# Performance work log

Measured on AMD Instinct MI355X. Metric: run time of the kernel, lower is better.

## Reference

```python
import jax, jax.numpy as jnp
import numpy as np

B, S, C, H, L = 256, 8, 8, 501, 56


def _lin_init(k, out_dim, in_dim):
    k1, k2 = jax.random.split(k)
    s = 1.0 / np.sqrt(in_dim)
    w = jax.random.uniform(k1, (out_dim, in_dim), jnp.float32, -s, s)
    b = jax.random.uniform(k2, (out_dim,), jnp.float32, -s, s)
    return w, b


def setup_inputs() -> dict:
    key = jax.random.key(0)
    ks = jax.random.split(key, 12)
    lin1_w, lin1_b = _lin_init(ks[0], H, L)
    av_w1, av_b1 = _lin_init(ks[1], 2 * H, H)
    av_w2, av_b2 = _lin_init(ks[2], C, 2 * H)
    ae_w1, ae_b1 = _lin_init(ks[3], 4 * H, 2 * H)
    ae_w2, ae_b2 = _lin_init(ks[4], 1, 4 * H)
    gate_w, gate_b = _lin_init(ks[5], H, H)
    map_w, map_b = _lin_init(ks[6], H, H)
    gru_w_ih, gru_b_ih = _lin_init(ks[7], 3 * H, C)
    gru_w_hh, gru_b_hh = _lin_init(ks[8], 3 * H, H)
    z = jax.random.normal(ks[9], (B, L), jnp.float32)
    dep_graph = jax.random.uniform(ks[10], (B, S, S), jnp.float32)
    node_encoding = jax.random.uniform(ks[11], (B, S, C), jnp.float32)
    return dict(z=z, dep_graph=dep_graph, node_encoding=node_encoding,
                lin1_w=lin1_w, lin1_b=lin1_b,
                av_w1=av_w1, av_b1=av_b1, av_w2=av_w2, av_b2=av_b2,
                ae_w1=ae_w1, ae_b1=ae_b1, ae_w2=ae_w2, ae_b2=ae_b2,
                gate_w=gate_w, gate_b=gate_b, map_w=map_w, map_b=map_b,
                gru_w_ih=gru_w_ih, gru_w_hh=gru_w_hh,
                gru_b_ih=gru_b_ih, gru_b_hh=gru_b_hh)


def _forward(z, dep_graph, node_encoding,
             lin1_w, lin1_b, av_w1, av_b1, av_w2, av_b2,
             ae_w1, ae_b1, ae_w2, ae_b2, gate_w, gate_b, map_w, map_b,
             gru_w_ih, gru_w_hh, gru_b_ih, gru_b_hh):
    b, s, _ = dep_graph.shape
    h = lin1_w.shape[0]

    def gru(x, hid):  # torch GRUCell math
        gi = x @ gru_w_ih.T + gru_b_ih
        gh = hid @ gru_w_hh.T + gru_b_hh
        i_r, i_z, i_n = jnp.split(gi, 3, axis=-1)
        h_r, h_z, h_n = jnp.split(gh, 3, axis=-1)
        r = jax.nn.sigmoid(i_r + h_r)
        zz = jax.nn.sigmoid(i_z + h_z)
        n = jnp.tanh(i_n + r * h_n)
        return (1.0 - zz) * n + zz * hid

    pos = jnp.arange(s)

    def outer_step(carry, xs):
        graph_state, nhs = carry  # (B,H), (B,S,H)
        index, x, dep_row = xs    # scalar, (B,C), (B,S)
        logits = jax.nn.softmax(
            jax.nn.relu(graph_state @ av_w1.T + av_b1) @ av_w2.T + av_b2, axis=-1)
        # index==0: gru seeded with graph_state; otherwise zero hidden
        h0 = jnp.where(index == 0, graph_state, jnp.zeros_like(graph_state))
        hv0 = gru(x, h0)

        def inner_step(c, j):
            hv, nhs_c, edge_row = c
            active = j < index  # replicate range(index-1, -1, -1)
            hidden_j = nhs_c[:, j]
            e = jnp.concatenate([hv, hidden_j], axis=1)
            edge = (jax.nn.relu(e @ ae_w1.T + ae_b1) @ ae_w2.T + ae_b2)[:, 0]
            edge_row = edge_row.at[:, j].set(jnp.where(active, edge, 0.0))
            # ancestors: dep_graph[:, index] with positions < j zeroed
            anc = dep_row * (pos >= j).astype(dep_row.dtype)
            a = (nhs_c * anc[:, :, None]).reshape(b * s, h)
            h_in = (jax.nn.sigmoid(a @ gate_w.T + gate_b) *
                    (a @ map_w.T + map_b)).reshape(b, s, h).sum(axis=1)
            hv_new = gru(x, h_in)
            hv = jnp.where(active, hv_new, hv)
            nhs_c = nhs_c.at[:, index].set(jnp.where(active, hv_new, nhs_c[:, index]))
            return (hv, nhs_c, edge_row), None

        (hv, nhs, edge_row), _ = jax.lax.scan(
            inner_step, (hv0, nhs, jnp.zeros((b, s), dep_graph.dtype)),
            jnp.arange(s - 1, -1, -1))
        nhs = nhs.at[:, index].set(hv)
        return (hv, nhs), (logits, edge_row)

    graph_state0 = z @ lin1_w.T + lin1_b
    nhs0 = jnp.zeros((b, s, h), z.dtype)
    (_, _), (gen_enc, gen_dep) = jax.lax.scan(
        outer_step, (graph_state0, nhs0),
        (jnp.arange(s), node_encoding.transpose(1, 0, 2), dep_graph.transpose(1, 0, 2)))
    return gen_dep.transpose(1, 0, 2), gen_enc.transpose(1, 0, 2)


def reference(z, dep_graph, node_encoding,
              lin1_w, lin1_b, av_w1, av_b1, av_w2, av_b2,
              ae_w1, ae_b1, ae_w2, ae_b2, gate_w, gate_b, map_w, map_b,
              gru_w_ih, gru_w_hh, gru_b_ih, gru_b_hh):
    return _forward(z, dep_graph, node_encoding,
                    lin1_w, lin1_b, av_w1, av_b1, av_w2, av_b2,
                    ae_w1, ae_b1, ae_w2, ae_b2, gate_w, gate_b, map_w, map_b,
                    gru_w_ih, gru_w_hh, gru_b_ih, gru_b_hh)
```

## Files before the change

kernel.cpp:

```cpp
#include <hip/hip_runtime.h>
#include <math.h>

constexpr int NB  = 256;
constexpr int NS  = 8;
constexpr int NC  = 8;
constexpr int NH  = 501;
constexpr int NL  = 56;
constexpr int NH2 = 1002;
constexpr int NH3 = 1503;
constexpr int NH4 = 2004;
constexpr int KT  = 1536;
constexpr int KE  = 512;
constexpr int KA  = 1024;
constexpr int HV  = 512 * 256;

typedef unsigned short u16;
typedef short bf16x8v __attribute__((ext_vector_type(8)));
typedef _Float16 f16x8v __attribute__((ext_vector_type(8)));
typedef _Float16 f16x4v __attribute__((ext_vector_type(4)));
typedef float f32x4 __attribute__((ext_vector_type(4)));

__device__ __forceinline__ float sigf(float x) { return 1.0f / (1.0f + __expf(-x)); }
__device__ __forceinline__ float tanh2(float x) { return 2.0f * sigf(2.0f * x) - 1.0f; }

__device__ __forceinline__ u16 f2bf(float x) {
  union { float f; unsigned u; } c; c.f = x;
  unsigned r = (c.u + 0x7fffu + ((c.u >> 16) & 1u)) >> 16;
  return (u16)r;
}
__device__ __forceinline__ float bf2f(u16 h) {
  union { float f; unsigned u; } c; c.u = ((unsigned)h) << 16; return c.f;
}

__device__ __forceinline__ void async_copy16(const void* g, void* l) {
  __builtin_amdgcn_global_load_lds(
      (const __attribute__((address_space(1))) unsigned int*)g,
      (__attribute__((address_space(3))) unsigned int*)l, 16, 0, 0);
}

__device__ __forceinline__ f32x4 mfma_bf(bf16x8v a, bf16x8v b, f32x4 c) {
  return __builtin_amdgcn_mfma_f32_16x16x32_bf16(a, b, c, 0, 0, 0);
}
__device__ __forceinline__ f32x4 mfma_h(f16x8v a, f16x8v b, f32x4 c) {
  return __builtin_amdgcn_mfma_f32_16x16x32_f16(a, b, c, 0, 0, 0);
}

__device__ __forceinline__ void storeTrio(u16* __restrict__ T, int b, int h0, const float v[4]) {
  size_t base = (size_t)b * KT;
  if (h0 + 3 < NH) {
    ushort4 hi4, lo4;
    u16 hi, lo;
    hi = f2bf(v[0]); lo = f2bf(v[0] - bf2f(hi)); hi4.x = hi; lo4.x = lo;
    hi = f2bf(v[1]); lo = f2bf(v[1] - bf2f(hi)); hi4.y = hi; lo4.y = lo;
    hi = f2bf(v[2]); lo = f2bf(v[2] - bf2f(hi)); hi4.z = hi; lo4.z = lo;
    hi = f2bf(v[3]); lo = f2bf(v[3] - bf2f(hi)); hi4.w = hi; lo4.w = lo;
    *(ushort4*)&T[base + h0]        = hi4;
    *(ushort4*)&T[base + 512 + h0]  = lo4;
    *(ushort4*)&T[base + 1024 + h0] = hi4;
  } else {
    for (int r = 0; r < 4; ++r) {
      int h = h0 + r;
      if (h < NH) {
        u16 hi = f2bf(v[r]); u16 lo = f2bf(v[r] - bf2f(hi));
        T[base + h] = hi; T[base + 512 + h] = lo; T[base + 1024 + h] = hi;
      }
    }
  }
}

__global__ __launch_bounds__(256) void kPack(
    const float* __restrict__ gate_w, const float* __restrict__ map_w,
    const float* __restrict__ w_hh, const float* __restrict__ av_w1,
    const float* __restrict__ ae_w1,
    u16* __restrict__ Wgm, u16* __restrict__ Whh, u16* __restrict__ Wav1,
    _Float16* __restrict__ Wlr) {
  int r = blockIdx.x;
  if (r < 3584) {
    for (int k = threadIdx.x; k < 512; k += 256) {
      float v = 0.f; u16* dst; int rr;
      if (r < 1024) {
        int h = (r < 512) ? r : r - 512;
        if (h < NH && k < NH) v = (r < 512) ? gate_w[h * NH + k] : map_w[h * NH + k];
        dst = Wgm; rr = r;
      } else if (r < 2560) {
        rr = r - 1024; int g = rr >> 9, h = rr & 511;
        if (h < NH && k < NH) v = w_hh[((size_t)g * NH + h) * NH + k];
        dst = Whh;
      } else {
        rr = r - 2560;
        if (rr < NH2 && k < NH) v = av_w1[(size_t)rr * NH + k];
        dst = Wav1;
      }
      u16 hi = f2bf(v); u16 lo = f2bf(v - bf2f(hi));
      dst[(size_t)rr * KT + k] = hi;
      dst[(size_t)rr * KT + 512 + k] = hi;
      dst[(size_t)rr * KT + 1024 + k] = lo;
    }
  } else {
    int m = r - 3584;
    for (int k = threadIdx.x; k < KA; k += 256) {
      float v = 0.f;
      if (m < NH4) {
        if (k < 512) { if (k < NH) v = ae_w1[(size_t)m * NH2 + k]; }
        else { int kk = k - 512; if (kk < NH) v = ae_w1[(size_t)m * NH2 + NH + kk]; }
      }
      Wlr[(size_t)m * KA + k] = (_Float16)v;
    }
  }
}

__global__ __launch_bounds__(256) void kInit(
    float* __restrict__ out0, const float* __restrict__ ae_b2,
    u16* __restrict__ trio, _Float16* __restrict__ Xe, _Float16* __restrict__ Xn,
    const float* __restrict__ z, const float* __restrict__ lin1_w,
    const float* __restrict__ lin1_b, float* __restrict__ g0,
    const float* __restrict__ ne, const float* __restrict__ w_ih,
    const float* __restrict__ b_ih, float* __restrict__ giN, float* __restrict__ giT) {
  int blk = blockIdx.x, t = threadIdx.x;
  if (blk < 64) {
    int e = blk * 256 + t;
    int b = e >> 6, r = e & 63;
    int i = r >> 3, jj = r & 7;
    out0[b * 64 + i * 8 + jj] = (jj < i) ? ae_b2[0] : 0.f;
  } else if (blk < 75) {
    u16* T = trio + (size_t)(blk - 64) * ((size_t)NB * KT) + (size_t)t * KT;
#pragma unroll
    for (int seg = 0; seg < 3; ++seg)
      for (int h = NH; h < 512; ++h) T[seg * 512 + h] = 0;
  } else if (blk < 103) {
    _Float16* X = Xe + (size_t)(blk - 75) * NB * KE + (size_t)t * KE;
    for (int h = NH; h < 512; ++h) X[h] = (_Float16)0.f;
  } else if (blk < 110) {
    _Float16* X = Xn + (size_t)(blk - 103) * NB * KE + (size_t)t * KE;
    for (int h = NH; h < 512; ++h) X[h] = (_Float16)0.f;
  } else if (blk < 366) {
    int b = blk - 110;
    const float* zr = z + (size_t)b * NL;
    for (int h = t; h < NH; h += 256) {
      const float* wr = lin1_w + (size_t)h * NL;
      float acc = lin1_b[h];
#pragma unroll
      for (int l = 0; l < NL; ++l) acc += zr[l] * wr[l];
      g0[h * NB + b] = acc;
      u16 hi = f2bf(acc), lo = f2bf(acc - bf2f(hi));
      trio[(size_t)b * KT + h] = hi;
      trio[(size_t)b * KT + 512 + h] = lo;
      trio[(size_t)b * KT + 1024 + h] = hi;
    }
  } else {
    int r0 = (blk - 366) * 6, b = t;
    for (int rr = 0; rr < 6; ++rr) {
      int r = r0 + rr;
      if (r >= NH3) break;
      int g = (r >= NH2) ? 2 : ((r >= NH) ? 1 : 0);
      int h = r - g * NH;
      float wv[8];
#pragma unroll
      for (int c = 0; c < 8; ++c) wv[c] = w_ih[r * NC + c];
      float bb = b_ih[r];
      for (int idx = 0; idx < 8; ++idx) {
        float acc = bb;
#pragma unroll
        for (int c = 0; c < 8; ++c) acc += ne[b * 64 + idx * 8 + c] * wv[c];
        giN[((size_t)idx * NH3 + r) * NB + b] = acc;
        giT[((size_t)idx * NB + b) * KT + g * 512 + h] = acc;
      }
    }
  }
}


__global__ __launch_bounds__(512) void kGMT(
    const u16* __restrict__ Wgm, const u16* __restrict__ Bsrc,
    float* __restrict__ PcO, float* __restrict__ QcO,
    const float* __restrict__ dep, const float* __restrict__ gate_b,
    const float* __restrict__ map_b, float* __restrict__ RS, u16* __restrict__ hinT,
    const float* __restrict__ giT, const float* __restrict__ b_hh,
    _Float16* __restrict__ Xe0, int index) {
  __shared__ f32x4 red[8 * 4 * 64];
  const int b = blockIdx.x, t = threadIdx.x, w = t >> 6, l = t & 63;
  const int quad = l >> 4, lan = l & 15;
  const int ht = b & 31, ct = b >> 5;
  const u16* Ag = Wgm + (size_t)(ht * 16 + lan) * KT;
  const u16* Am = Wgm + (size_t)(512 + ht * 16 + lan) * KT;
  const u16* B0 = Bsrc + (size_t)(ct * 32 + lan) * KT;
  const u16* B1 = Bsrc + (size_t)(ct * 32 + 16 + lan) * KT;
  const int kb = w * 192 + quad * 8;
  f32x4 a0 = {0.f,0.f,0.f,0.f}, a1 = a0, a2 = a0, a3 = a0;
#pragma unroll 3
  for (int ks = 0; ks < 6; ++ks) {
    int k = kb + ks * 32;
    bf16x8v bg = *(const bf16x8v*)&B0[k];
    bf16x8v bh = *(const bf16x8v*)&B1[k];
    bf16x8v ag = *(const bf16x8v*)&Ag[k];
    bf16x8v am = *(const bf16x8v*)&Am[k];
    a0 = mfma_bf(ag, bg, a0); a1 = mfma_bf(ag, bh, a1);
    a2 = mfma_bf(am, bg, a2); a3 = mfma_bf(am, bh, a3);
  }
  red[(w * 4 + 0) * 64 + l] = a0;
  red[(w * 4 + 1) * 64 + l] = a1;
  red[(w * 4 + 2) * 64 + l] = a2;
  red[(w * 4 + 3) * 64 + l] = a3;
  __syncthreads();
  if (w < 2) {
    int ns = w;
    f32x4 G = red[(0 * 4 + ns) * 64 + l];
    f32x4 M = red[(0 * 4 + 2 + ns) * 64 + l];
#pragma unroll
    for (int p = 1; p < 8; ++p) {
      G += red[(p * 4 + ns) * 64 + l];
      M += red[(p * 4 + 2 + ns) * 64 + l];
    }
    int c = ct * 32 + ns * 16 + lan;
    int h0 = ht * 16 + quad * 4;
    int j = index - 1;
    float dj = dep[c * 64 + index * 8 + j];
    float vout[4];
#pragma unroll
    for (int reg = 0; reg < 4; ++reg) {
      int h = h0 + reg; float v = 0.f;
      if (h < NH) {
        PcO[h * NB + c] = G[reg];
        QcO[h * NB + c] = M[reg];
        float gb = gate_b[h], mb = map_b[h];
        float kbv = sigf(gb) * mb;
        float fj = sigf(dj * G[reg] + gb) * (dj * M[reg] + mb);
        RS[h * NB + c] = fj;
        v = fj + 7.0f * kbv;
      }
      vout[reg] = v;
    }
    storeTrio(hinT, c, h0, vout);
  } else if (w < 4) {
    int t2 = t - 128;
    int c = ct * 32 + (t2 & 31);
    int hb = t2 >> 5;
    const float* g = giT + ((size_t)index * NB + c) * KT;
#pragma unroll
    for (int k = 0; k < 4; ++k) {
      int h = ht * 16 + hb * 4 + k;
      if (h < NH) {
        float rr = sigf(g[h] + b_hh[h]);
        float zz = sigf(g[512 + h] + b_hh[NH + h]);
        float nn = tanh2(g[1024 + h] + rr * b_hh[2 * NH + h]);
        Xe0[(size_t)c * KE + h] = (_Float16)((1.f - zz) * nn);
      }
    }
  }
}

__global__ __launch_bounds__(512) void kGM0(
    const u16* __restrict__ Wgm, const u16* __restrict__ Bsrc,
    const float* __restrict__ dep, const float* __restrict__ gate_b,
    const float* __restrict__ map_b,
    const float* __restrict__ Pcj, const float* __restrict__ Qcj,
    float* __restrict__ RS, u16* __restrict__ hinT, int index, int j) {
  __shared__ f32x4 red[8 * 4 * 64];
  const int b = blockIdx.x, t = threadIdx.x, w = t >> 6, l = t & 63;
  const int quad = l >> 4, lan = l & 15;
  const int ht = b & 31, ct = b >> 5;
  const u16* Ag = Wgm + (size_t)(ht * 16 + lan) * KT;
  const u16* Am = Wgm + (size_t)(512 + ht * 16 + lan) * KT;
  const u16* B0 = Bsrc + (size_t)(ct * 32 + lan) * KT;
  const u16* B1 = Bsrc + (size_t)(ct * 32 + 16 + lan) * KT;
  const int kb = w * 192 + quad * 8;
  f32x4 a0 = {0.f,0.f,0.f,0.f}, a1 = a0, a2 = a0, a3 = a0;
#pragma unroll 3
  for (int ks = 0; ks < 6; ++ks) {
    int k = kb + ks * 32;
    bf16x8v bg = *(const bf16x8v*)&B0[k];
    bf16x8v bh = *(const bf16x8v*)&B1[k];
    bf16x8v ag = *(const bf16x8v*)&Ag[k];
    bf16x8v am = *(const bf16x8v*)&Am[k];
    a0 = mfma_bf(ag, bg, a0); a1 = mfma_bf(ag, bh, a1);
    a2 = mfma_bf(am, bg, a2); a3 = mfma_bf(am, bh, a3);
  }
  red[(w * 4 + 0) * 64 + l] = a0;
  red[(w * 4 + 1) * 64 + l] = a1;
  red[(w * 4 + 2) * 64 + l] = a2;
  red[(w * 4 + 3) * 64 + l] = a3;
  __syncthreads();
  if (w < 2) {
    int ns = w;
    f32x4 G = red[(0 * 4 + ns) * 64 + l];
    f32x4 M = red[(0 * 4 + 2 + ns) * 64 + l];
#pragma unroll
    for (int p = 1; p < 8; ++p) {
      G += red[(p * 4 + ns) * 64 + l];
      M += red[(p * 4 + 2 + ns) * 64 + l];
    }
    int c = ct * 32 + ns * 16 + lan;
    int h0 = ht * 16 + quad * 4;
    float dj = dep[c * 64 + index * 8 + j];
    float di = dep[c * 64 + index * 8 + index];
    float cnt = (float)(7 - (index - j));
    float vout[4];
#pragma unroll
    for (int reg = 0; reg < 4; ++reg) {
      int h = h0 + reg; float v = 0.f;
      if (h < NH) {
        float gb = gate_b[h], mb = map_b[h];
        float kbv = sigf(gb) * mb;
        float fj = sigf(dj * Pcj[h * NB + c] + gb) * (dj * Qcj[h * NB + c] + mb);
        float rs = RS[h * NB + c] + fj;
        RS[h * NB + c] = rs;
        float fi = sigf(di * G[reg] + gb) * (di * M[reg] + mb);
        v = rs + fi + cnt * kbv;
      }
      vout[reg] = v;
    }
    storeTrio(hinT, c, h0, vout);
  }
}

__global__ __launch_bounds__(512) void kHHw(
    const u16* __restrict__ Whh, const u16* __restrict__ Bsrc,
    const float* __restrict__ hidF, const float* __restrict__ gi,
    const float* __restrict__ b_hh,
    u16* __restrict__ dstT, _Float16* __restrict__ XeSlot, _Float16* __restrict__ XnSlot) {
  __shared__ f32x4 red[8 * 6 * 64];
  const int b = blockIdx.x, t = threadIdx.x, w = t >> 6, l = t & 63;
  const int quad = l >> 4, lan = l & 15;
  const int ht = b & 31, ct = b >> 5;
  const u16* Ar = Whh + (size_t)(ht * 16 + lan) * KT;
  const u16* Az = Whh + (size_t)(512 + ht * 16 + lan) * KT;
  const u16* An = Whh + (size_t)(1024 + ht * 16 + lan) * KT;
  const u16* B0 = Bsrc + (size_t)(ct * 32 + lan) * KT;
  const u16* B1 = Bsrc + (size_t)(ct * 32 + 16 + lan) * KT;
  const int kb = w * 192 + quad * 8;
  f32x4 r0 = {0.f,0.f,0.f,0.f}, r1 = r0, z0 = r0, z1 = r0, n0 = r0, n1 = r0;
#pragma unroll 3
  for (int ks = 0; ks < 6; ++ks) {
    int k = kb + ks * 32;
    bf16x8v bg = *(const bf16x8v*)&B0[k];
    bf16x8v bh = *(const bf16x8v*)&B1[k];
    bf16x8v ar = *(const bf16x8v*)&Ar[k];
    bf16x8v az = *(const bf16x8v*)&Az[k];
    bf16x8v an = *(const bf16x8v*)&An[k];
    r0 = mfma_bf(ar, bg, r0); r1 = mfma_bf(ar, bh, r1);
    z0 = mfma_bf(az, bg, z0); z1 = mfma_bf(az, bh, z1);
    n0 = mfma_bf(an, bg, n0); n1 = mfma_bf(an, bh, n1);
  }
  red[(w * 6 + 0) * 64 + l] = r0;
  red[(w * 6 + 1) * 64 + l] = r1;
  red[(w * 6 + 2) * 64 + l] = z0;
  red[(w * 6 + 3) * 64 + l] = z1;
  red[(w * 6 + 4) * 64 + l] = n0;
  red[(w * 6 + 5) * 64 + l] = n1;
  __syncthreads();
  if (w < 2) {
    int ns = w;
    f32x4 Rr = red[(0 * 6 + 0 + ns) * 64 + l];
    f32x4 Rz = red[(0 * 6 + 2 + ns) * 64 + l];
    f32x4 Rn = red[(0 * 6 + 4 + ns) * 64 + l];
#pragma unroll
    for (int p = 1; p < 8; ++p) {
      Rr += red[(p * 6 + 0 + ns) * 64 + l];
      Rz += red[(p * 6 + 2 + ns) * 64 + l];
      Rn += red[(p * 6 + 4 + ns) * 64 + l];
    }
    int c = ct * 32 + ns * 16 + lan;
    int h0 = ht * 16 + quad * 4;
    float vout[4];
#pragma unroll
    for (int reg = 0; reg < 4; ++reg) {
      int h = h0 + reg; float v = 0.f;
      if (h < NH) {
        float ir = gi[h * NB + c];
        float iz = gi[(NH + h) * NB + c];
        float inn = gi[(2 * NH + h) * NB + c];
        float rr = sigf(ir + Rr[reg] + b_hh[h]);
        float zz = sigf(iz + Rz[reg] + b_hh[NH + h]);
        float nn = tanh2(inn + rr * (Rn[reg] + b_hh[2 * NH + h]));
        float hd;
        if (hidF) hd = hidF[h * NB + c];
        else hd = bf2f(Bsrc[(size_t)c * KT + h]) + bf2f(Bsrc[(size_t)c * KT + 512 + h]);
        v = (1.f - zz) * nn + zz * hd;
      }
      vout[reg] = v;
    }
    storeTrio(dstT, c, h0, vout);
    if (XeSlot || XnSlot) {
      if (h0 + 3 < NH) {
        f16x4v xv; xv[0] = (_Float16)vout[0]; xv[1] = (_Float16)vout[1];
        xv[2] = (_Float16)vout[2]; xv[3] = (_Float16)vout[3];
        if (XeSlot) *(f16x4v*)&XeSlot[(size_t)c * KE + h0] = xv;
        if (XnSlot) *(f16x4v*)&XnSlot[(size_t)c * KE + h0] = xv;
      } else {
        for (int reg = 0; reg < 4; ++reg)
          if (h0 + reg < NH) {
            if (XeSlot) XeSlot[(size_t)c * KE + h0 + reg] = (_Float16)vout[reg];
            if (XnSlot) XnSlot[(size_t)c * KE + h0 + reg] = (_Float16)vout[reg];
          }
      }
    }
  }
}


__global__ __launch_bounds__(256) void kEdge(const _Float16* __restrict__ Wlr,
                                             const _Float16* __restrict__ Xe,
                                             const _Float16* __restrict__ Xn,
                                             const float* __restrict__ ae_b1,
                                             const float* __restrict__ ae_w2,
                                             float* __restrict__ out0) {
  __shared__ u16 sA[2][128 * 32];
  __shared__ u16 sB[2][128 * 32];
  __shared__ float shW[4][8][16];
  const int t = threadIdx.x, w = t >> 6, l = t & 63, quad = l >> 4, lan = l & 15;
  const int mB = blockIdx.x * 128, nB0 = blockIdx.y * 128;
  const int qs = quad ^ ((lan >> 1) & 3);
  const int sseg = (l & 3) ^ ((l >> 3) & 3);
  int sid = blockIdx.y >> 1;
  int idec = 1, bse = 0;
  while (sid >= bse + idec) { bse += idec; idec++; }
  int jdec = idec - 1 - (sid - bse);
  int r0 = (w * 2 + 0) * 16 + (l >> 2), r1 = (w * 2 + 1) * 16 + (l >> 2);
  const _Float16* gA0 = Wlr + (size_t)(mB + r0) * KA + sseg * 8;
  const _Float16* gA1 = Wlr + (size_t)(mB + r1) * KA + sseg * 8;
  const _Float16* Xe0 = Xe + (size_t)(nB0 + r0) * KE + sseg * 8;
  const _Float16* Xe1 = Xe + (size_t)(nB0 + r1) * KE + sseg * 8;
  const _Float16* Xn0 = Xn + ((size_t)jdec * NB + ((nB0 + r0) & 255)) * KE + sseg * 8;
  const _Float16* Xn1 = Xn + ((size_t)jdec * NB + ((nB0 + r1) & 255)) * KE + sseg * 8;
  f32x4 acc[2][8];
#pragma unroll
  for (int mt = 0; mt < 2; ++mt)
#pragma unroll
    for (int ns = 0; ns < 8; ++ns) acc[mt][ns] = (f32x4){0.f,0.f,0.f,0.f};
  async_copy16(gA0, &sA[0][(w * 2 + 0) * 512]);
  async_copy16(gA1, &sA[0][(w * 2 + 1) * 512]);
  async_copy16(Xe0, &sB[0][(w * 2 + 0) * 512]);
  async_copy16(Xe1, &sB[0][(w * 2 + 1) * 512]);
  for (int c = 0; c < 32; ++c) {
    __syncthreads();
    if (c + 1 < 32) {
      int nb = (c + 1) & 1, cc = c + 1;
      async_copy16(gA0 + cc * 32, &sA[nb][(w * 2 + 0) * 512]);
      async_copy16(gA1 + cc * 32, &sA[nb][(w * 2 + 1) * 512]);
      const _Float16* b0 = (cc < 16) ? (Xe0 + cc * 32) : (Xn0 + (cc - 16) * 32);
      const _Float16* b1 = (cc < 16) ? (Xe1 + cc * 32) : (Xn1 + (cc - 16) * 32);
      async_copy16(b0, &sB[nb][(w * 2 + 0) * 512]);
      async_copy16(b1, &sB[nb][(w * 2 + 1) * 512]);
    }
    const u16* bufA = sA[c & 1];
    const u16* bufB = sB[c & 1];
    f16x8v av[2];
#pragma unroll
    for (int mt = 0; mt < 2; ++mt)
      av[mt] = *(const f16x8v*)&bufA[(w * 32 + mt * 16 + lan) * 32 + qs * 8];
#pragma unroll
    for (int ns = 0; ns < 8; ++ns) {
      f16x8v bv = *(const f16x8v*)&bufB[(ns * 16 + lan) * 32 + qs * 8];
#pragma unroll
      for (int mt = 0; mt < 2; ++mt) acc[mt][ns] = mfma_h(av[mt], bv, acc[mt][ns]);
    }
  }
  float b1v[2][4], w2v[2][4];
#pragma unroll
  for (int mt = 0; mt < 2; ++mt) {
    int m0 = mB + w * 32 + mt * 16 + quad * 4;
#pragma unroll
    for (int reg = 0; reg < 4; ++reg) {
      int m = m0 + reg;
      b1v[mt][reg] = (m < NH4) ? ae_b1[m] : 0.f;
      w2v[mt][reg] = (m < NH4) ? ae_w2[m] : 0.f;
    }
  }
#pragma unroll
  for (int ns = 0; ns < 8; ++ns) {
    float s = 0.f;
#pragma unroll
    for (int mt = 0; mt < 2; ++mt) {
#pragma unroll
      for (int reg = 0; reg < 4; ++reg) {
        float v = acc[mt][ns][reg] + b1v[mt][reg];
        if (v > 0.f) s += v * w2v[mt][reg];
      }
    }
    s += __shfl_xor(s, 16);
    s += __shfl_xor(s, 32);
    if (quad == 0) shW[w][ns][lan] = s;
  }
  __syncthreads();
  if (t < 128) {
    int ns = t >> 4, ln = t & 15;
    float tot = shW[0][ns][ln] + shW[1][ns][ln] + shW[2][ns][ln] + shW[3][ns][ln];
    int b = (nB0 + ln + ns * 16) & 255;
    atomicAdd(&out0[b * 64 + idec * 8 + jdec], tot);
  }
}

__global__ __launch_bounds__(256) void kLogA(const u16* __restrict__ Wav1,
                                             const u16* __restrict__ Bsrc,
                                             const float* __restrict__ av_b1,
                                             _Float16* __restrict__ t1) {
  __shared__ u16 sA[2][64 * 32];
  __shared__ u16 sB[2][128 * 32];
  const int t = threadIdx.x, w = t >> 6, l = t & 63, quad = l >> 4, lan = l & 15;
  const int mB = blockIdx.x * 64, nB0 = blockIdx.y * 128;
  const int qs = quad ^ ((lan >> 1) & 3);
  const int sseg = (l & 3) ^ ((l >> 3) & 3);
  int rA = w * 16 + (l >> 2);
  int r0 = (w * 2 + 0) * 16 + (l >> 2), r1 = (w * 2 + 1) * 16 + (l >> 2);
  const u16* gA = Wav1 + (size_t)(mB + rA) * KT + sseg * 8;
  const u16* gB0 = Bsrc + (size_t)(nB0 + r0) * KT + sseg * 8;
  const u16* gB1 = Bsrc + (size_t)(nB0 + r1) * KT + sseg * 8;
  f32x4 acc[8];
#pragma unroll
  for (int ns = 0; ns < 8; ++ns) acc[ns] = (f32x4){0.f,0.f,0.f,0.f};
  async_copy16(gA, &sA[0][w * 512]);
  async_copy16(gB0, &sB[0][(w * 2 + 0) * 512]);
  async_copy16(gB1, &sB[0][(w * 2 + 1) * 512]);
  for (int c = 0; c < 48; ++c) {
    __syncthreads();
    if (c + 1 < 48) {
      int nb = (c + 1) & 1, off = (c + 1) * 32;
      async_copy16(gA + off, &sA[nb][w * 512]);
      async_copy16(gB0 + off, &sB[nb][(w * 2 + 0) * 512]);
      async_copy16(gB1 + off, &sB[nb][(w * 2 + 1) * 512]);
    }
    const u16* bufA = sA[c & 1];
    const u16* bufB = sB[c & 1];
    bf16x8v av = *(const bf16x8v*)&bufA[(w * 16 + lan) * 32 + qs * 8];
#pragma unroll
    for (int ns = 0; ns < 8; ++ns) {
      bf16x8v bv = *(const bf16x8v*)&bufB[(ns * 16 + lan) * 32 + qs * 8];
      acc[ns] = mfma_bf(av, bv, acc[ns]);
    }
  }
#pragma unroll
  for (int ns = 0; ns < 8; ++ns) {
    int col = nB0 + ns * 16 + lan;
    int m0 = mB + w * 16 + quad * 4;
    f16x4v rv;
#pragma unroll
    for (int reg = 0; reg < 4; ++reg) {
      int m = m0 + reg;
      float v = acc[ns][reg] + ((m < NH2) ? av_b1[m] : 0.f);
      rv[reg] = (_Float16)(v > 0.f ? v : 0.f);
    }
    *(f16x4v*)&t1[(size_t)col * 1024 + m0] = rv;
  }
}

__global__ __launch_bounds__(256) void kSoft(const _Float16* __restrict__ t1,
                                             const float* __restrict__ av_w2,
                                             const float* __restrict__ av_b2,
                                             float* __restrict__ out1) {
  const int t = threadIdx.x, w = t >> 6, l = t & 63;
  int col = blockIdx.x * 4 + w;
  const _Float16* trow = t1 + (size_t)col * 1024;
  float s[8] = {};
  for (int i = 0; i < 16; ++i) {
    int k = i * 64 + l;
    if (k < NH2) {
      float v = (float)trow[k];
#pragma unroll
      for (int c = 0; c < 8; ++c) s[c] += v * av_w2[c * NH2 + k];
    }
  }
#pragma unroll
  for (int c = 0; c < 8; ++c) {
    s[c] += __shfl_xor(s[c], 32);
    s[c] += __shfl_xor(s[c], 16);
    s[c] += __shfl_xor(s[c], 8);
    s[c] += __shfl_xor(s[c], 4);
    s[c] += __shfl_xor(s[c], 2);
    s[c] += __shfl_xor(s[c], 1);
  }
  if (l == 0) {
    float lg[8], mx = -1e30f;
#pragma unroll
    for (int c = 0; c < 8; ++c) { lg[c] = s[c] + av_b2[c]; mx = fmaxf(mx, lg[c]); }
    float den = 0.f;
#pragma unroll
    for (int c = 0; c < 8; ++c) den += __expf(lg[c] - mx);
    int idx = col >> 8, b = col & 255;
#pragma unroll
    for (int c = 0; c < 8; ++c)
      out1[(b * NS + idx) * NC + c] = __expf(lg[c] - mx) / den;
  }
}


extern "C" void kernel_launch(void* const* d_in, const int* in_sizes, int n_in,
                              void* d_out, int out_size, void* d_ws, size_t ws_size,
                              hipStream_t stream) {
  (void)in_sizes; (void)n_in; (void)out_size; (void)ws_size;
  const float* z      = (const float*)d_in[0];
  const float* dep    = (const float*)d_in[1];
  const float* ne     = (const float*)d_in[2];
  const float* lin1_w = (const float*)d_in[3];
  const float* lin1_b = (const float*)d_in[4];
  const float* av_w1  = (const float*)d_in[5];
  const float* av_b1  = (const float*)d_in[6];
  const float* av_w2  = (const float*)d_in[7];
  const float* av_b2  = (const float*)d_in[8];
  const float* ae_w1  = (const float*)d_in[9];
  const float* ae_b1  = (const float*)d_in[10];
  const float* ae_w2  = (const float*)d_in[11];
  const float* ae_b2  = (const float*)d_in[12];
  const float* gate_w = (const float*)d_in[13];
  const float* gate_b = (const float*)d_in[14];
  const float* map_w  = (const float*)d_in[15];
  const float* map_b  = (const float*)d_in[16];
  const float* w_ih   = (const float*)d_in[17];
  const float* w_hh   = (const float*)d_in[18];
  const float* b_ih   = (const float*)d_in[19];
  const float* b_hh   = (const float*)d_in[20];

  float* out0 = (float*)d_out;
  float* out1 = out0 + NB * NS * NS;

  const size_t SLOT = (size_t)NB * KT;
  char* p = (char*)d_ws;
  u16* trio = (u16*)p;            p += 11 * SLOT * 2;
  _Float16* Xe = (_Float16*)p;    p += (size_t)28 * NB * KE * 2;
  _Float16* Xn = (_Float16*)p;    p += (size_t)7 * NB * KE * 2;
  u16* Wgm  = (u16*)p;            p += (size_t)1024 * KT * 2;
  u16* Whh  = (u16*)p;            p += (size_t)1536 * KT * 2;
  u16* Wav1 = (u16*)p;            p += (size_t)1024 * KT * 2;
  _Float16* Wlr = (_Float16*)p;   p += (size_t)2048 * KA * 2;
  _Float16* t1 = (_Float16*)p;    p += (size_t)2048 * 1024 * 2;
  float* Pc   = (float*)p;        p += (size_t)8 * HV * 4;
  float* Qc   = (float*)p;        p += (size_t)8 * HV * 4;
  float* RS   = (float*)p;        p += (size_t)HV * 4;
  float* g0   = (float*)p;        p += (size_t)HV * 4;
  float* giN  = (float*)p;        p += (size_t)8 * NH3 * NB * 4;
  float* giT  = (float*)p;        p += (size_t)8 * NB * KT * 4;

  u16* hinT = trio + 8 * SLOT;

  kPack<<<5632, 256, 0, stream>>>(gate_w, map_w, w_hh, av_w1, ae_w1, Wgm, Whh, Wav1, Wlr);
  kInit<<<617, 256, 0, stream>>>(out0, ae_b2, trio, Xe, Xn,
                                 z, lin1_w, lin1_b, g0, ne, w_ih, b_ih, giN, giT);

  kHHw<<<256, 512, 0, stream>>>(Whh, trio, g0, giN, b_hh,
                                trio + 1 * SLOT, nullptr, Xn);

  for (int i = 0; i <= 6; ++i) {
    int index = i + 1;
    int sid0 = index * (index - 1) / 2;
    const float* gi_i = giN + (size_t)index * NH3 * NB;
    kGMT<<<256, 512, 0, stream>>>(Wgm, trio + (size_t)(i + 1) * SLOT,
                                  Pc + (size_t)i * HV, Qc + (size_t)i * HV,
                                  dep, gate_b, map_b, RS, hinT, giT, b_hh,
                                  Xe + (size_t)sid0 * NB * KE, index);
    bool final1 = (index == 1);
    u16* dst = final1 ? (trio + 2 * SLOT) : (trio + 9 * SLOT);
    kHHw<<<256, 512, 0, stream>>>(Whh, hinT, nullptr, gi_i, b_hh, dst,
        (index - 1 > 0) ? (Xe + (size_t)(sid0 + 1) * NB * KE) : nullptr,
        final1 ? (Xn + (size_t)1 * NB * KE) : nullptr);
    u16* prev = dst;
    int par = 1;
    for (int j = index - 2; j >= 0; --j) {
      kGM0<<<256, 512, 0, stream>>>(Wgm, prev, dep, gate_b, map_b,
                                    Pc + (size_t)j * HV, Qc + (size_t)j * HV,
                                    RS, hinT, index, j);
      bool fin = (j == 0);
      u16* d2 = (fin && index <= 6) ? (trio + (size_t)(index + 1) * SLOT)
                                    : (trio + (size_t)(9 + par) * SLOT);
      kHHw<<<256, 512, 0, stream>>>(Whh, hinT, nullptr, gi_i, b_hh, d2,
          (j > 0) ? (Xe + (size_t)(sid0 + index - j) * NB * KE) : nullptr,
          (fin && index <= 6) ? (Xn + (size_t)index * NB * KE) : nullptr);
      prev = d2; par ^= 1;
    }
  }

  kLogA<<<dim3(16, 16), 256, 0, stream>>>(Wav1, trio, av_b1, t1);
  kSoft<<<512, 256, 0, stream>>>(t1, av_w2, av_b2, out1);
  kEdge<<<dim3(16, 56), 256, 0, stream>>>(Wlr, Xe, Xn, ae_b1, ae_w2, out0);
}
```

Measured before the change: 861.0 us.

## Fuse per-index GRU/gate kernel chain into one persistent kernel with grid barriers

```diff
diff --git a/kernel.cpp b/kernel.cpp
--- a/kernel.cpp
+++ b/kernel.cpp
@@ -30,6 +30,32 @@
 }
 __device__ __forceinline__ float bf2f(u16 h) {
   union { float f; unsigned u; } c; c.u = ((unsigned)h) << 16; return c.f;
+}
+
+__device__ __forceinline__ unsigned sc_ld(const unsigned* p) {
+  return __hip_atomic_load(p, __ATOMIC_RELAXED, __HIP_MEMORY_SCOPE_AGENT);
+}
+__device__ __forceinline__ void sc_st(unsigned* p, unsigned v) {
+  __hip_atomic_store(p, v, __ATOMIC_RELAXED, __HIP_MEMORY_SCOPE_AGENT);
+}
+__device__ __forceinline__ bf16x8v sc_ld16(const u16* p) {
+  union { unsigned u[4]; bf16x8v v; } r;
+  const unsigned* q = (const unsigned*)p;
+  r.u[0] = sc_ld(q); r.u[1] = sc_ld(q + 1); r.u[2] = sc_ld(q + 2); r.u[3] = sc_ld(q + 3);
+  return r.v;
+}
+
+__device__ __forceinline__ void ctSync(unsigned* flag, int tid) {
+  __syncthreads();
+  if (tid == 0) {
+    __hip_atomic_fetch_add(flag, 1u, __ATOMIC_RELEASE, __HIP_MEMORY_SCOPE_AGENT);
+    int guard = 0;
+    while (__hip_atomic_load(flag, __ATOMIC_RELAXED, __HIP_MEMORY_SCOPE_AGENT) < 32u) {
+      __builtin_amdgcn_s_sleep(2);
+      if (++guard > (1 << 22)) break;
+    }
+  }
+  __syncthreads();
 }
 
 __device__ __forceinline__ void async_copy16(const void* g, void* l) {
@@ -65,6 +91,29 @@
         T[base + h] = hi; T[base + 512 + h] = lo; T[base + 1024 + h] = hi;
       }
     }
+  }
+}
+
+__device__ __forceinline__ void storeTrioSC(u16* __restrict__ T, int b, int h0, const float v[4]) {
+  size_t base = (size_t)b * KT;
+  if (h0 + 3 < NH) {
+    union { ushort4 s; unsigned u[2]; } hi4, lo4;
+    u16 hi, lo;
+    hi = f2bf(v[0]); lo = f2bf(v[0] - bf2f(hi)); hi4.s.x = hi; lo4.s.x = lo;
+    hi = f2bf(v[1]); lo = f2bf(v[1] - bf2f(hi)); hi4.s.y = hi; lo4.s.y = lo;
+    hi = f2bf(v[2]); lo = f2bf(v[2] - bf2f(hi)); hi4.s.z = hi; lo4.s.z = lo;
+    hi = f2bf(v[3]); lo = f2bf(v[3] - bf2f(hi)); hi4.s.w = hi; lo4.s.w = lo;
+    unsigned* p0 = (unsigned*)&T[base + h0];
+    unsigned* p1 = (unsigned*)&T[base + 512 + h0];
+    unsigned* p2 = (unsigned*)&T[base + 1024 + h0];
+    sc_st(p0, hi4.u[0]); sc_st(p0 + 1, hi4.u[1]);
+    sc_st(p1, lo4.u[0]); sc_st(p1 + 1, lo4.u[1]);
+    sc_st(p2, hi4.u[0]); sc_st(p2 + 1, hi4.u[1]);
+  } else if (h0 < NH) {
+    u16 hi = f2bf(v[0]); u16 lo = f2bf(v[0] - bf2f(hi));
+    sc_st((unsigned*)&T[base + h0], (unsigned)hi);
+    sc_st((unsigned*)&T[base + 512 + h0], (unsigned)lo);
+    sc_st((unsigned*)&T[base + 1024 + h0], (unsigned)hi);
   }
 }
 
@@ -115,7 +164,8 @@
     const float* __restrict__ z, const float* __restrict__ lin1_w,
     const float* __restrict__ lin1_b, float* __restrict__ g0,
     const float* __restrict__ ne, const float* __restrict__ w_ih,
-    const float* __restrict__ b_ih, float* __restrict__ giN, float* __restrict__ giT) {
+    const float* __restrict__ b_ih, float* __restrict__ giN, float* __restrict__ giT,
+    unsigned* __restrict__ flags) {
   int blk = blockIdx.x, t = threadIdx.x;
   if (blk < 64) {
     int e = blk * 256 + t;
@@ -147,7 +197,7 @@
       trio[(size_t)b * KT + 512 + h] = lo;
       trio[(size_t)b * KT + 1024 + h] = hi;
     }
-  } else {
+  } else if (blk < 617) {
     int r0 = (blk - 366) * 6, b = t;
     for (int rr = 0; rr < 6; ++rr) {
       int r = r0 + rr;
@@ -166,18 +216,19 @@
         giT[((size_t)idx * NB + b) * KT + g * 512 + h] = acc;
       }
     }
-  }
-}
-
-
-__global__ __launch_bounds__(512) void kGMT(
+  } else {
+    for (int i = t; i < 2048; i += 256) flags[i] = 0u;
+  }
+}
+
+
+__device__ __forceinline__ void phaseGMT(
     const u16* __restrict__ Wgm, const u16* __restrict__ Bsrc,
     float* __restrict__ PcO, float* __restrict__ QcO,
     const float* __restrict__ dep, const float* __restrict__ gate_b,
     const float* __restrict__ map_b, float* __restrict__ RS, u16* __restrict__ hinT,
     const float* __restrict__ giT, const float* __restrict__ b_hh,
-    _Float16* __restrict__ Xe0, int index) {
-  __shared__ f32x4 red[8 * 4 * 64];
+    _Float16* __restrict__ Xe0, int index, f32x4* red) {
   const int b = blockIdx.x, t = threadIdx.x, w = t >> 6, l = t & 63;
   const int quad = l >> 4, lan = l & 15;
   const int ht = b & 31, ct = b >> 5;
@@ -230,7 +281,7 @@
       }
       vout[reg] = v;
     }
-    storeTrio(hinT, c, h0, vout);
+    storeTrioSC(hinT, c, h0, vout);
   } else if (w < 4) {
     int t2 = t - 128;
     int c = ct * 32 + (t2 & 31);
@@ -249,13 +300,12 @@
   }
 }
 
-__global__ __launch_bounds__(512) void kGM0(
+__device__ __forceinline__ void phaseGM0(
     const u16* __restrict__ Wgm, const u16* __restrict__ Bsrc,
     const float* __restrict__ dep, const float* __restrict__ gate_b,
     const float* __restrict__ map_b,
     const float* __restrict__ Pcj, const float* __restrict__ Qcj,
-    float* __restrict__ RS, u16* __restrict__ hinT, int index, int j) {
-  __shared__ f32x4 red[8 * 4 * 64];
+    float* __restrict__ RS, u16* __restrict__ hinT, int index, int j, f32x4* red) {
   const int b = blockIdx.x, t = threadIdx.x, w = t >> 6, l = t & 63;
   const int quad = l >> 4, lan = l & 15;
   const int ht = b & 31, ct = b >> 5;
@@ -268,8 +318,8 @@
 #pragma unroll 3
   for (int ks = 0; ks < 6; ++ks) {
     int k = kb + ks * 32;
-    bf16x8v bg = *(const bf16x8v*)&B0[k];
-    bf16x8v bh = *(const bf16x8v*)&B1[k];
+    bf16x8v bg = sc_ld16(&B0[k]);
+    bf16x8v bh = sc_ld16(&B1[k]);
     bf16x8v ag = *(const bf16x8v*)&Ag[k];
     bf16x8v am = *(const bf16x8v*)&Am[k];
     a0 = mfma_bf(ag, bg, a0); a1 = mfma_bf(ag, bh, a1);
@@ -309,7 +359,131 @@
       }
       vout[reg] = v;
     }
-    storeTrio(hinT, c, h0, vout);
+    storeTrioSC(hinT, c, h0, vout);
+  }
+}
+
+__device__ __forceinline__ void phaseHH(
+    const u16* __restrict__ Whh, const u16* __restrict__ Bsrc,
+    const float* __restrict__ gi, const float* __restrict__ b_hh,
+    u16* __restrict__ dstT, _Float16* __restrict__ XeSlot, _Float16* __restrict__ XnSlot,
+    f32x4* red) {
+  const int b = blockIdx.x, t = threadIdx.x, w = t >> 6, l = t & 63;
+  const int quad = l >> 4, lan = l & 15;
+  const int ht = b & 31, ct = b >> 5;
+  const u16* Ar = Whh + (size_t)(ht * 16 + lan) * KT;
+  const u16* Az = Whh + (size_t)(512 + ht * 16 + lan) * KT;
+  const u16* An = Whh + (size_t)(1024 + ht * 16 + lan) * KT;
+  const u16* B0 = Bsrc + (size_t)(ct * 32 + lan) * KT;
+  const u16* B1 = Bsrc + (size_t)(ct * 32 + 16 + lan) * KT;
+  const int kb = w * 192 + quad * 8;
+  f32x4 r0 = {0.f,0.f,0.f,0.f}, r1 = r0, z0 = r0, z1 = r0, n0 = r0, n1 = r0;
+#pragma unroll 3
+  for (int ks = 0; ks < 6; ++ks) {
+    int k = kb + ks * 32;
+    bf16x8v bg = sc_ld16(&B0[k]);
+    bf16x8v bh = sc_ld16(&B1[k]);
+    bf16x8v ar = *(const bf16x8v*)&Ar[k];
+    bf16x8v az = *(const bf16x8v*)&Az[k];
+    bf16x8v an = *(const bf16x8v*)&An[k];
+    r0 = mfma_bf(ar, bg, r0); r1 = mfma_bf(ar, bh, r1);
+    z0 = mfma_bf(az, bg, z0); z1 = mfma_bf(az, bh, z1);
+    n0 = mfma_bf(an, bg, n0); n1 = mfma_bf(an, bh, n1);
+  }
+  red[(w * 6 + 0) * 64 + l] = r0;
+  red[(w * 6 + 1) * 64 + l] = r1;
+  red[(w * 6 + 2) * 64 + l] = z0;
+  red[(w * 6 + 3) * 64 + l] = z1;
+  red[(w * 6 + 4) * 64 + l] = n0;
+  red[(w * 6 + 5) * 64 + l] = n1;
+  __syncthreads();
+  if (w < 2) {
+    int ns = w;
+    f32x4 Rr = red[(0 * 6 + 0 + ns) * 64 + l];
+    f32x4 Rz = red[(0 * 6 + 2 + ns) * 64 + l];
+    f32x4 Rn = red[(0 * 6 + 4 + ns) * 64 + l];
+#pragma unroll
+    for (int p = 1; p < 8; ++p) {
+      Rr += red[(p * 6 + 0 + ns) * 64 + l];
+      Rz += red[(p * 6 + 2 + ns) * 64 + l];
+      Rn += red[(p * 6 + 4 + ns) * 64 + l];
+    }
+    int c = ct * 32 + ns * 16 + lan;
+    int h0 = ht * 16 + quad * 4;
+    union { unsigned u[2]; ushort4 s; } HI, LO;
+    const unsigned* ph = (const unsigned*)&Bsrc[(size_t)c * KT + h0];
+    HI.u[0] = sc_ld(ph); HI.u[1] = sc_ld(ph + 1);
+    const unsigned* pl = (const unsigned*)&Bsrc[(size_t)c * KT + 512 + h0];
+    LO.u[0] = sc_ld(pl); LO.u[1] = sc_ld(pl + 1);
+    u16 hiv[4] = {HI.s.x, HI.s.y, HI.s.z, HI.s.w};
+    u16 lov[4] = {LO.s.x, LO.s.y, LO.s.z, LO.s.w};
+    float vout[4];
+#pragma unroll
+    for (int reg = 0; reg < 4; ++reg) {
+      int h = h0 + reg; float v = 0.f;
+      if (h < NH) {
+        float ir = gi[h * NB + c];
+        float iz = gi[(NH + h) * NB + c];
+        float inn = gi[(2 * NH + h) * NB + c];
+        float rr = sigf(ir + Rr[reg] + b_hh[h]);
+        float zz = sigf(iz + Rz[reg] + b_hh[NH + h]);
+        float nn = tanh2(inn + rr * (Rn[reg] + b_hh[2 * NH + h]));
+        float hd = bf2f(hiv[reg]) + bf2f(lov[reg]);
+        v = (1.f - zz) * nn + zz * hd;
+      }
+      vout[reg] = v;
+    }
+    storeTrioSC(dstT, c, h0, vout);
+    if (XeSlot || XnSlot) {
+      for (int reg = 0; reg < 4; ++reg)
+        if (h0 + reg < NH) {
+          if (XeSlot) XeSlot[(size_t)c * KE + h0 + reg] = (_Float16)vout[reg];
+          if (XnSlot) XnSlot[(size_t)c * KE + h0 + reg] = (_Float16)vout[reg];
+        }
+    }
+  }
+}
+
+__global__ __launch_bounds__(512) void kStep(
+    const u16* __restrict__ Wgm, const u16* __restrict__ Whh,
+    const u16* __restrict__ GSin, u16* __restrict__ GSout,
+    u16* __restrict__ hinT, u16* __restrict__ hvA, u16* __restrict__ hvB,
+    float* __restrict__ PcI, float* __restrict__ QcI,
+    const float* __restrict__ PcAll, const float* __restrict__ QcAll,
+    const float* __restrict__ dep, const float* __restrict__ gate_b,
+    const float* __restrict__ map_b, float* __restrict__ RS,
+    const float* __restrict__ giT, const float* __restrict__ gi,
+    const float* __restrict__ b_hh,
+    _Float16* __restrict__ XeBase, _Float16* __restrict__ XnSlot,
+    unsigned* __restrict__ flags, int index) {
+  __shared__ f32x4 red[8 * 6 * 64];
+  const int tid = threadIdx.x;
+  const int ct = blockIdx.x >> 5;
+  int fphase = 0;
+
+  phaseGMT(Wgm, GSin, PcI, QcI, dep, gate_b, map_b, RS, hinT, giT, b_hh,
+           XeBase, index, red);
+  ctSync(&flags[(fphase++) * 8 + ct], tid);
+
+  {
+    u16* dst = (index == 1) ? GSout : hvA;
+    _Float16* xe = (index > 1) ? (XeBase + (size_t)1 * NB * KE) : nullptr;
+    _Float16* xn = (index == 1) ? XnSlot : nullptr;
+    phaseHH(Whh, hinT, gi, b_hh, dst, xe, xn, red);
+  }
+  const u16* prev = hvA;
+  int par = 1;
+  for (int j = index - 2; j >= 0; --j) {
+    ctSync(&flags[(fphase++) * 8 + ct], tid);
+    phaseGM0(Wgm, prev, dep, gate_b, map_b,
+             PcAll + (size_t)j * HV, QcAll + (size_t)j * HV, RS, hinT, index, j, red);
+    ctSync(&flags[(fphase++) * 8 + ct], tid);
+    bool fin = (j == 0);
+    u16* d2 = (fin && index <= 6) ? GSout : (par ? hvB : hvA);
+    phaseHH(Whh, hinT, gi, b_hh, d2,
+            (j > 0) ? (XeBase + (size_t)(index - j) * NB * KE) : nullptr,
+            fin ? XnSlot : nullptr, red);
+    prev = d2; par ^= 1;
   }
 }
 
@@ -317,7 +491,7 @@
     const u16* __restrict__ Whh, const u16* __restrict__ Bsrc,
     const float* __restrict__ hidF, const float* __restrict__ gi,
     const float* __restrict__ b_hh,
-    u16* __restrict__ dstT, _Float16* __restrict__ XeSlot, _Float16* __restrict__ XnSlot) {
+    u16* __restrict__ dstT, _Float16* __restrict__ XnSlot) {
   __shared__ f32x4 red[8 * 6 * 64];
   const int b = blockIdx.x, t = threadIdx.x, w = t >> 6, l = t & 63;
   const int quad = l >> 4, lan = l & 15;
@@ -372,28 +546,15 @@
         float rr = sigf(ir + Rr[reg] + b_hh[h]);
         float zz = sigf(iz + Rz[reg] + b_hh[NH + h]);
         float nn = tanh2(inn + rr * (Rn[reg] + b_hh[2 * NH + h]));
-        float hd;
-        if (hidF) hd = hidF[h * NB + c];
-        else hd = bf2f(Bsrc[(size_t)c * KT + h]) + bf2f(Bsrc[(size_t)c * KT + 512 + h]);
+        float hd = hidF[h * NB + c];
         v = (1.f - zz) * nn + zz * hd;
       }
       vout[reg] = v;
     }
     storeTrio(dstT, c, h0, vout);
-    if (XeSlot || XnSlot) {
-      if (h0 + 3 < NH) {
-        f16x4v xv; xv[0] = (_Float16)vout[0]; xv[1] = (_Float16)vout[1];
-        xv[2] = (_Float16)vout[2]; xv[3] = (_Float16)vout[3];
-        if (XeSlot) *(f16x4v*)&XeSlot[(size_t)c * KE + h0] = xv;
-        if (XnSlot) *(f16x4v*)&XnSlot[(size_t)c * KE + h0] = xv;
-      } else {
-        for (int reg = 0; reg < 4; ++reg)
-          if (h0 + reg < NH) {
-            if (XeSlot) XeSlot[(size_t)c * KE + h0 + reg] = (_Float16)vout[reg];
-            if (XnSlot) XnSlot[(size_t)c * KE + h0 + reg] = (_Float16)vout[reg];
-          }
-      }
-    }
+    for (int reg = 0; reg < 4; ++reg)
+      if (h0 + reg < NH)
+        XnSlot[(size_t)c * KE + h0 + reg] = (_Float16)vout[reg];
   }
 }
 
@@ -628,43 +789,32 @@
   float* g0   = (float*)p;        p += (size_t)HV * 4;
   float* giN  = (float*)p;        p += (size_t)8 * NH3 * NB * 4;
   float* giT  = (float*)p;        p += (size_t)8 * NB * KT * 4;
+  unsigned* flags = (unsigned*)p; p += (size_t)2048 * 4;
 
   u16* hinT = trio + 8 * SLOT;
+  u16* hvA  = trio + 9 * SLOT;
+  u16* hvB  = trio + 10 * SLOT;
 
   kPack<<<5632, 256, 0, stream>>>(gate_w, map_w, w_hh, av_w1, ae_w1, Wgm, Whh, Wav1, Wlr);
-  kInit<<<617, 256, 0, stream>>>(out0, ae_b2, trio, Xe, Xn,
-                                 z, lin1_w, lin1_b, g0, ne, w_ih, b_ih, giN, giT);
-
-  kHHw<<<256, 512, 0, stream>>>(Whh, trio, g0, giN, b_hh,
-                                trio + 1 * SLOT, nullptr, Xn);
-
-  for (int i = 0; i <= 6; ++i) {
-    int index = i + 1;
+  kInit<<<618, 256, 0, stream>>>(out0, ae_b2, trio, Xe, Xn,
+                                 z, lin1_w, lin1_b, g0, ne, w_ih, b_ih, giN, giT, flags);
+
+  kHHw<<<256, 512, 0, stream>>>(Whh, trio, g0, giN, b_hh, trio + 1 * SLOT, Xn);
+
+  for (int index = 1; index <= 7; ++index) {
     int sid0 = index * (index - 1) / 2;
-    const float* gi_i = giN + (size_t)index * NH3 * NB;
-    kGMT<<<256, 512, 0, stream>>>(Wgm, trio + (size_t)(i + 1) * SLOT,
-                                  Pc + (size_t)i * HV, Qc + (size_t)i * HV,
-                                  dep, gate_b, map_b, RS, hinT, giT, b_hh,
-                                  Xe + (size_t)sid0 * NB * KE, index);
-    bool final1 = (index == 1);
-    u16* dst = final1 ? (trio + 2 * SLOT) : (trio + 9 * SLOT);
-    kHHw<<<256, 512, 0, stream>>>(Whh, hinT, nullptr, gi_i, b_hh, dst,
-        (index - 1 > 0) ? (Xe + (size_t)(sid0 + 1) * NB * KE) : nullptr,
-        final1 ? (Xn + (size_t)1 * NB * KE) : nullptr);
-    u16* prev = dst;
-    int par = 1;
-    for (int j = index - 2; j >= 0; --j) {
-      kGM0<<<256, 512, 0, stream>>>(Wgm, prev, dep, gate_b, map_b,
-                                    Pc + (size_t)j * HV, Qc + (size_t)j * HV,
-                                    RS, hinT, index, j);
-      bool fin = (j == 0);
-      u16* d2 = (fin && index <= 6) ? (trio + (size_t)(index + 1) * SLOT)
-                                    : (trio + (size_t)(9 + par) * SLOT);
-      kHHw<<<256, 512, 0, stream>>>(Whh, hinT, nullptr, gi_i, b_hh, d2,
-          (j > 0) ? (Xe + (size_t)(sid0 + index - j) * NB * KE) : nullptr,
-          (fin && index <= 6) ? (Xn + (size_t)index * NB * KE) : nullptr);
-      prev = d2; par ^= 1;
-    }
+    kStep<<<256, 512, 0, stream>>>(
+        Wgm, Whh,
+        trio + (size_t)index * SLOT,
+        trio + (size_t)((index <= 6) ? (index + 1) : 9) * SLOT,
+        hinT, hvA, hvB,
+        Pc + (size_t)(index - 1) * HV, Qc + (size_t)(index - 1) * HV,
+        Pc, Qc,
+        dep, gate_b, map_b, RS, giT,
+        giN + (size_t)index * NH3 * NB, b_hh,
+        Xe + (size_t)sid0 * NB * KE,
+        (index <= 6) ? (Xn + (size_t)index * NB * KE) : nullptr,
+        flags + (size_t)index * 128, index);
   }
 
   kLogA<<<dim3(16, 16), 256, 0, stream>>>(Wav1, trio, av_b1, t1);
```

New measurement: 2.057 ms. 139% more time.
